# Kernel optimization log

Hardware: AMD Instinct MI355X
Metric: run time of the kernel (lower is better)

## Reference

```python
import jax, jax.numpy as jnp
import numpy as np

B, L, D = 16, 2048, 320          # batch, frames, stacked feature dim (80 mel * 4 reduction)
CODEBOOK_SIZE, CODEBOOK_DIM = 8192, 16


def setup_inputs() -> dict:
    key = jax.random.key(0)
    k1, k2, k3 = jax.random.split(key, 3)
    masked_target_values = jax.random.normal(k1, (B, L, D), dtype=jnp.float32)
    # xavier_uniform_ for shape (D, codebook_dim): bound = sqrt(6/(fan_in+fan_out))
    bound = np.sqrt(6.0 / (D + CODEBOOK_DIM)).astype(np.float32)
    project_mat = jax.random.uniform(k2, (D, CODEBOOK_DIM), dtype=jnp.float32,
                                     minval=-bound, maxval=bound)
    cb = jax.random.normal(k3, (CODEBOOK_SIZE, CODEBOOK_DIM), dtype=jnp.float32)
    codebook_norm = cb / jnp.maximum(jnp.linalg.norm(cb, axis=-1, keepdims=True), 1e-12)
    return {"masked_target_values": masked_target_values,
            "project_mat": project_mat,
            "codebook_norm": codebook_norm}


def reference(masked_target_values, project_mat, codebook_norm):
    # project: (B, L, D) @ (D, K) -> (B, L, K)
    targets = jnp.einsum('bld,dk->blk', masked_target_values, project_mat)
    # L2 normalize along last dim (torch F.normalize with eps=1e-12)
    targets_norm = targets / jnp.maximum(
        jnp.linalg.norm(targets, axis=-1, keepdims=True), 1e-12)
    x2 = jnp.sum(targets_norm * targets_norm, axis=-1, keepdims=True)      # (B, L, 1)
    c2 = jnp.sum(codebook_norm * codebook_norm, axis=-1)                   # (C,)
    xc = jnp.einsum('blk,ck->blc', targets_norm, codebook_norm)            # (B, L, C)
    d2 = jnp.maximum(x2 + c2[None, None, :] - 2.0 * xc, 0.0)
    vector_distances = jnp.sqrt(d2)
    labels = jnp.argmin(vector_distances, axis=-1)                         # (B, L) int
    return labels
```

## Files before the change

### kernel.cpp

```cpp
#include <hip/hip_runtime.h>
#include <cfloat>

#define TOKENS 32768
#define DIM    320
#define NCODE  8192
#define NSPLIT 8
#define SPAN   (NCODE / NSPLIT)
#define NTILE  (SPAN / 32)
#define CERT_UNITS 32u
#define FBWAVES 2048
#define PROW   20

typedef __attribute__((ext_vector_type(8)))  short short8;
typedef __attribute__((ext_vector_type(16))) float f32x16;
typedef unsigned short ushort_t;
typedef unsigned int   uint_t;

static __device__ __forceinline__ ushort_t f2bf(float f) {
    uint_t u = __float_as_uint(f);
    u += 0x7fffu + ((u >> 16) & 1u);
    return (ushort_t)(u >> 16);
}
static __device__ __forceinline__ float bf2f(ushort_t h) {
    return __uint_as_float(((uint_t)h) << 16);
}
static __device__ __forceinline__ uint_t pack2(ushort_t a, ushort_t b) {
    return (uint_t)a | ((uint_t)b << 16);
}
static __device__ __forceinline__ uint_t umaxu(uint_t a, uint_t b) { return a > b ? a : b; }
static __device__ __forceinline__ uint_t uminu(uint_t a, uint_t b) { return a < b ? a : b; }

__global__ __launch_bounds__(256) void prep_kernel(
    const float* __restrict__ x,
    const float* __restrict__ P,
    const float* __restrict__ cb,
    float* __restrict__ tn,
    float* __restrict__ x2o,
    float* __restrict__ c2o,
    ushort_t* __restrict__ tnpack,
    ushort_t* __restrict__ cbpack,
    int* __restrict__ cnt)
{
    __shared__ float Ps[DIM * PROW];
    int bid = blockIdx.x, tid = threadIdx.x;
    if (bid < TOKENS / 32) {
        const float4* P4 = (const float4*)P;
        #pragma unroll
        for (int i = 0; i < 5; ++i) {
            int idx = tid + i * 256;
            int row = idx >> 2, col = idx & 3;
            *(float4*)(Ps + row * PROW + col * 4) = P4[idx];
        }
        __syncthreads();

        int sub = tid & 7;
        int tok = bid * 32 + (tid >> 3);
        const float* xr = x + (size_t)tok * DIM;
        float acc[16];
        #pragma unroll
        for (int k = 0; k < 16; ++k) acc[k] = 0.f;

        for (int i = 0; i < 40; ++i) {
            int d = i * 8 + sub;
            float xv = xr[d];
            const float4* pr = (const float4*)(Ps + d * PROW);
            float4 p0 = pr[0], p1 = pr[1], p2 = pr[2], p3 = pr[3];
            acc[0] = fmaf(xv, p0.x, acc[0]);   acc[1] = fmaf(xv, p0.y, acc[1]);
            acc[2] = fmaf(xv, p0.z, acc[2]);   acc[3] = fmaf(xv, p0.w, acc[3]);
            acc[4] = fmaf(xv, p1.x, acc[4]);   acc[5] = fmaf(xv, p1.y, acc[5]);
            acc[6] = fmaf(xv, p1.z, acc[6]);   acc[7] = fmaf(xv, p1.w, acc[7]);
            acc[8] = fmaf(xv, p2.x, acc[8]);   acc[9] = fmaf(xv, p2.y, acc[9]);
            acc[10] = fmaf(xv, p2.z, acc[10]); acc[11] = fmaf(xv, p2.w, acc[11]);
            acc[12] = fmaf(xv, p3.x, acc[12]); acc[13] = fmaf(xv, p3.y, acc[13]);
            acc[14] = fmaf(xv, p3.z, acc[14]); acc[15] = fmaf(xv, p3.w, acc[15]);
        }
        #pragma unroll
        for (int m = 1; m <= 4; m <<= 1) {
            #pragma unroll
            for (int k = 0; k < 16; ++k)
                acc[k] += __shfl_xor(acc[k], m);
        }
        float ss = 0.f;
        #pragma unroll
        for (int k = 0; k < 16; ++k) ss = fmaf(acc[k], acc[k], ss);
        float nrm = fmaxf(sqrtf(ss), 1e-12f);
        float inv = 1.0f / nrm;
        float t[16];
        #pragma unroll
        for (int k = 0; k < 16; ++k) t[k] = acc[k] * inv;
        float xx = 0.f;
        #pragma unroll
        for (int k = 0; k < 16; ++k) xx = fmaf(t[k], t[k], xx);

        ushort_t hi[16], lo[16];
        #pragma unroll
        for (int k = 0; k < 16; ++k) {
            hi[k] = f2bf(t[k]);
            lo[k] = f2bf(t[k] - bf2f(hi[k]));
        }
        if (sub < 4) {
            float4* tf = (float4*)(tn + (size_t)tok * 16);
            tf[sub] = make_float4(t[4 * sub], t[4 * sub + 1],
                                  t[4 * sub + 2], t[4 * sub + 3]);
        }
        uint4* dst = (uint4*)(tnpack + (size_t)tok * 32);
        if (sub == 4) dst[0] = make_uint4(pack2(hi[0], hi[1]), pack2(hi[2], hi[3]),
                                          pack2(hi[4], hi[5]), pack2(hi[6], hi[7]));
        if (sub == 5) dst[1] = make_uint4(pack2(hi[8], hi[9]), pack2(hi[10], hi[11]),
                                          pack2(hi[12], hi[13]), pack2(hi[14], hi[15]));
        if (sub == 6) dst[2] = make_uint4(pack2(lo[0], lo[1]), pack2(lo[2], lo[3]),
                                          pack2(lo[4], lo[5]), pack2(lo[6], lo[7]));
        if (sub == 7) dst[3] = make_uint4(pack2(lo[8], lo[9]), pack2(lo[10], lo[11]),
                                          pack2(lo[12], lo[13]), pack2(lo[14], lo[15]));
        if (sub == 0) x2o[tok] = xx;
    } else {
        int j = (bid - TOKENS / 32) * 256 + tid;
        const float4* cr4 = (const float4*)(cb + (size_t)j * 16);
        float4 c0 = cr4[0], c1 = cr4[1], c2v = cr4[2], c3 = cr4[3];
        float c[16] = {c0.x, c0.y, c0.z, c0.w, c1.x, c1.y, c1.z, c1.w,
                       c2v.x, c2v.y, c2v.z, c2v.w, c3.x, c3.y, c3.z, c3.w};
        float s = 0.f;
        #pragma unroll
        for (int k = 0; k < 16; ++k) s = fmaf(c[k], c[k], s);
        c2o[j] = s;
        ushort_t hi[16], lo[16];
        #pragma unroll
        for (int k = 0; k < 16; ++k) {
            hi[k] = f2bf(c[k]);
            lo[k] = f2bf(c[k] - bf2f(hi[k]));
        }
        uint4* dst = (uint4*)(cbpack + (size_t)j * 32);
        dst[0] = make_uint4(pack2(hi[0], hi[1]), pack2(hi[2], hi[3]),
                            pack2(hi[4], hi[5]), pack2(hi[6], hi[7]));
        dst[1] = make_uint4(pack2(hi[8], hi[9]), pack2(hi[10], hi[11]),
                            pack2(hi[12], hi[13]), pack2(hi[14], hi[15]));
        dst[2] = make_uint4(pack2(lo[0], lo[1]), pack2(lo[2], lo[3]),
                            pack2(lo[4], lo[5]), pack2(lo[6], lo[7]));
        dst[3] = make_uint4(pack2(lo[8], lo[9]), pack2(lo[10], lo[11]),
                            pack2(lo[12], lo[13]), pack2(lo[14], lo[15]));
        if (j == 0) cnt[0] = 0;
    }
}

__global__ __launch_bounds__(256, 4) void search_kernel(
    const ushort_t* __restrict__ tnpack,
    const ushort_t* __restrict__ cbpack,
    uint_t* __restrict__ pp1,
    uint_t* __restrict__ pp2)
{
    int lane = threadIdx.x & 63;
    int wave = threadIdx.x >> 6;
    int half = lane >> 5;
    int l31  = lane & 31;
    int split = blockIdx.y;
    int tbase = blockIdx.x * 128 + wave * 32;

    const ushort_t* tp = tnpack + (size_t)(tbase + l31) * 32;
    short8 hiA = *(const short8*)(tp + half * 8);
    short8 loA = *(const short8*)(tp + 16 + half * 8);

    f32x16 zero = {};
    uint_t p1[16], p2[16];
    #pragma unroll
    for (int r = 0; r < 16; ++r) { p1[r] = 0u; p2[r] = 0u; }

    for (int t = 0; t < NTILE; ++t) {
        int crow = split * SPAN + t * 32 + l31;
        const ushort_t* cp = cbpack + (size_t)crow * 32;
        short8 hiB = *(const short8*)(cp + half * 8);
        short8 loB = *(const short8*)(cp + 16 + half * 8);

        f32x16 acc = __builtin_amdgcn_mfma_f32_32x32x16_bf16(hiA, hiB, zero, 0, 0, 0);
        acc = __builtin_amdgcn_mfma_f32_32x32x16_bf16(loA, hiB, acc, 0, 0, 0);
        acc = __builtin_amdgcn_mfma_f32_32x32x16_bf16(hiA, loB, acc, 0, 0, 0);

        uint_t inv = 8191u - (uint_t)crow;
        #pragma unroll
        for (int r = 0; r < 16; ++r) {
            float kf = fmaf(acc[r], 131072.0f, 131072.0f);
            uint_t ku = (uint_t)kf;
            uint_t p  = (ku << 13) | inv;
            p2[r] = umaxu(p2[r], uminu(p, p1[r]));
            p1[r] = umaxu(p1[r], p);
        }
    }

    #pragma unroll
    for (int mask = 1; mask <= 16; mask <<= 1) {
        #pragma unroll
        for (int r = 0; r < 16; ++r) {
            uint_t a1 = (uint_t)__shfl_xor((int)p1[r], mask);
            uint_t a2 = (uint_t)__shfl_xor((int)p2[r], mask);
            uint_t np2 = umaxu(uminu(p1[r], a1), umaxu(p2[r], a2));
            p1[r] = umaxu(p1[r], a1);
            p2[r] = np2;
        }
    }

    #pragma unroll
    for (int r = 0; r < 16; ++r) {
        if (l31 == r) {
            int mrow = (r & 3) + 8 * (r >> 2) + 4 * half;
            size_t slot = (size_t)split * TOKENS + (tbase + mrow);
            pp1[slot] = p1[r];
            pp2[slot] = p2[r];
        }
    }
}

__global__ __launch_bounds__(256) void reduce_flag_kernel(
    const uint_t* __restrict__ pp1,
    const uint_t* __restrict__ pp2,
    int* __restrict__ out,
    int* __restrict__ cnt,
    int* __restrict__ flag)
{
    int tok = blockIdx.x * 256 + threadIdx.x;
    uint_t p1 = pp1[tok], p2 = pp2[tok];
    #pragma unroll
    for (int s = 1; s < NSPLIT; ++s) {
        uint_t a1 = pp1[(size_t)s * TOKENS + tok];
        uint_t a2 = pp2[(size_t)s * TOKENS + tok];
        uint_t np2 = umaxu(uminu(p1, a1), umaxu(p2, a2));
        p1 = umaxu(p1, a1);
        p2 = np2;
    }
    out[tok] = 8191 - (int)(p1 & 8191u);
    if ((p1 >> 13) - (p2 >> 13) <= CERT_UNITS) {
        int pz = atomicAdd(cnt, 1);
        flag[pz] = tok;
    }
}

__global__ __launch_bounds__(256) void fallback_kernel(
    const float* __restrict__ tn,
    const float* __restrict__ x2i,
    const float* __restrict__ cb,
    const float* __restrict__ c2i,
    const int* __restrict__ cnt,
    const int* __restrict__ flag,
    int* __restrict__ out)
{
    int lane = threadIdx.x & 63;
    int wid = blockIdx.x * 4 + (threadIdx.x >> 6);
    int n = cnt[0];
    for (int f = wid; f < n; f += FBWAVES) {
        int tok = flag[f];
        const float4* tr = (const float4*)(tn + (size_t)tok * 16);
        float4 t0 = tr[0], t1 = tr[1], t2 = tr[2], t3 = tr[3];
        float a[16] = {t0.x, t0.y, t0.z, t0.w, t1.x, t1.y, t1.z, t1.w,
                       t2.x, t2.y, t2.z, t2.w, t3.x, t3.y, t3.z, t3.w};
        float xx = x2i[tok];
        float mn = FLT_MAX;
        int   id = 0x7fffffff;

        int j = lane;
        const float4* c4p = (const float4*)(cb + (size_t)j * 16);
        float4 n0 = c4p[0], n1 = c4p[1], n2 = c4p[2], n3 = c4p[3];
        float ncc = c2i[j];

        for (int jj = 0; jj < 128; ++jj) {
            float4 c0 = n0, c1 = n1, c2v = n2, c3 = n3;
            float cc = ncc;
            int cj = j;
            j += 64;
            if (jj < 127) {
                const float4* nx = (const float4*)(cb + (size_t)j * 16);
                n0 = nx[0]; n1 = nx[1]; n2 = nx[2]; n3 = nx[3];
                ncc = c2i[j];
            }
            float dot = 0.f;
            dot = fmaf(a[0], c0.x, dot);   dot = fmaf(a[1], c0.y, dot);
            dot = fmaf(a[2], c0.z, dot);   dot = fmaf(a[3], c0.w, dot);
            dot = fmaf(a[4], c1.x, dot);   dot = fmaf(a[5], c1.y, dot);
            dot = fmaf(a[6], c1.z, dot);   dot = fmaf(a[7], c1.w, dot);
            dot = fmaf(a[8], c2v.x, dot);  dot = fmaf(a[9], c2v.y, dot);
            dot = fmaf(a[10], c2v.z, dot); dot = fmaf(a[11], c2v.w, dot);
            dot = fmaf(a[12], c3.x, dot);  dot = fmaf(a[13], c3.y, dot);
            dot = fmaf(a[14], c3.z, dot);  dot = fmaf(a[15], c3.w, dot);
            float e = fmaf(-2.f, dot, xx + cc);
            if (e < mn) { mn = e; id = cj; }
        }
        #pragma unroll
        for (int mask = 1; mask <= 32; mask <<= 1) {
            float pmn = __shfl_xor(mn, mask);
            int   pid = __shfl_xor(id, mask);
            bool take = (pmn < mn) || (pmn == mn && pid < id);
            if (take) { mn = pmn; id = pid; }
        }
        if (lane == 0) out[tok] = id;
    }
}

extern "C" void kernel_launch(void* const* d_in, const int* in_sizes, int n_in,
                              void* d_out, int out_size, void* d_ws, size_t ws_size,
                              hipStream_t stream) {
    const float* x   = (const float*)d_in[0];
    const float* P   = (const float*)d_in[1];
    const float* cbn = (const float*)d_in[2];

    float* ws = (float*)d_ws;
    float*  tn   = ws;
    float*  x2   = tn + (size_t)TOKENS * 16;
    float*  c2   = x2 + TOKENS;
    uint_t* pp1  = (uint_t*)(c2 + NCODE);
    uint_t* pp2  = pp1 + (size_t)NSPLIT * TOKENS;
    int*    flag = (int*)(pp2 + (size_t)NSPLIT * TOKENS);
    int*    cnt  = flag + TOKENS;
    ushort_t* tnpack = (ushort_t*)(cnt + 16);
    ushort_t* cbpack = tnpack + (size_t)TOKENS * 32;
    int* labels = (int*)d_out;

    prep_kernel<<<TOKENS / 32 + NCODE / 256, 256, 0, stream>>>(
        x, P, cbn, tn, x2, c2, tnpack, cbpack, cnt);
    dim3 sg(TOKENS / 128, NSPLIT);
    search_kernel<<<sg, 256, 0, stream>>>(tnpack, cbpack, pp1, pp2);
    reduce_flag_kernel<<<TOKENS / 256, 256, 0, stream>>>(pp1, pp2, labels, cnt, flag);
    fallback_kernel<<<FBWAVES / 4, 256, 0, stream>>>(tn, x2, cbn, c2, cnt, flag, labels);
}
```

Baseline: 190.0 us.

## Fuse projection, MFMA search, merge and fallback into one per-block kernel

Replaces the four-kernel pipeline (prep, split search, reduce/flag, global fallback) with a small codebook pack kernel plus one fused kernel. Each block of 32 tokens projects and normalizes them into shared memory, then its four waves each scan a quarter of the codebook with bf16 hi/lo MFMA. The per-wave partials are merged in shared memory, and ambiguous tokens are resolved with an exact fp32 scan by the same block. This removes the global intermediates, atomics and extra launches. In exchange, each block now reads the whole packed codebook, and the grid holds fewer waves per token. The in-block fallback is serialized with syncthreads and can stall blocks that have many flagged tokens.

```diff
diff --git a/kernel.cpp b/kernel.cpp
--- a/kernel.cpp
+++ b/kernel.cpp
@@ -4,12 +4,9 @@
 #define TOKENS 32768
 #define DIM    320
 #define NCODE  8192
-#define NSPLIT 8
-#define SPAN   (NCODE / NSPLIT)
-#define NTILE  (SPAN / 32)
+#define PROW   20
+#define NTILE  64
 #define CERT_UNITS 32u
-#define FBWAVES 2048
-#define PROW   20
 
 typedef __attribute__((ext_vector_type(8)))  short short8;
 typedef __attribute__((ext_vector_type(16))) float f32x16;
@@ -30,20 +27,58 @@
 static __device__ __forceinline__ uint_t umaxu(uint_t a, uint_t b) { return a > b ? a : b; }
 static __device__ __forceinline__ uint_t uminu(uint_t a, uint_t b) { return a < b ? a : b; }
 
-__global__ __launch_bounds__(256) void prep_kernel(
+__global__ __launch_bounds__(256) void pack_kernel(
+    const float* __restrict__ cb,
+    float* __restrict__ c2o,
+    ushort_t* __restrict__ cbpack)
+{
+    int j = blockIdx.x * 256 + threadIdx.x;
+    const float4* cr4 = (const float4*)(cb + (size_t)j * 16);
+    float4 c0 = cr4[0], c1 = cr4[1], c2v = cr4[2], c3 = cr4[3];
+    float c[16] = {c0.x, c0.y, c0.z, c0.w, c1.x, c1.y, c1.z, c1.w,
+                   c2v.x, c2v.y, c2v.z, c2v.w, c3.x, c3.y, c3.z, c3.w};
+    float s = 0.f;
+    #pragma unroll
+    for (int k = 0; k < 16; ++k) s = fmaf(c[k], c[k], s);
+    c2o[j] = s;
+    ushort_t hi[16], lo[16];
+    #pragma unroll
+    for (int k = 0; k < 16; ++k) {
+        hi[k] = f2bf(c[k]);
+        lo[k] = f2bf(c[k] - bf2f(hi[k]));
+    }
+    uint4* dst = (uint4*)(cbpack + (size_t)j * 32);
+    dst[0] = make_uint4(pack2(hi[0], hi[1]), pack2(hi[2], hi[3]),
+                        pack2(hi[4], hi[5]), pack2(hi[6], hi[7]));
+    dst[1] = make_uint4(pack2(hi[8], hi[9]), pack2(hi[10], hi[11]),
+                        pack2(hi[12], hi[13]), pack2(hi[14], hi[15]));
+    dst[2] = make_uint4(pack2(lo[0], lo[1]), pack2(lo[2], lo[3]),
+                        pack2(lo[4], lo[5]), pack2(lo[6], lo[7]));
+    dst[3] = make_uint4(pack2(lo[8], lo[9]), pack2(lo[10], lo[11]),
+                        pack2(lo[12], lo[13]), pack2(lo[14], lo[15]));
+}
+
+__global__ __launch_bounds__(256, 4) void fused_kernel(
     const float* __restrict__ x,
     const float* __restrict__ P,
     const float* __restrict__ cb,
-    float* __restrict__ tn,
-    float* __restrict__ x2o,
-    float* __restrict__ c2o,
-    ushort_t* __restrict__ tnpack,
-    ushort_t* __restrict__ cbpack,
-    int* __restrict__ cnt)
+    const float* __restrict__ c2g,
+    const ushort_t* __restrict__ cbpack,
+    int* __restrict__ out)
 {
     __shared__ float Ps[DIM * PROW];
-    int bid = blockIdx.x, tid = threadIdx.x;
-    if (bid < TOKENS / 32) {
+    __shared__ ushort_t ApackS[32 * 32];
+    __shared__ float tnS[32 * 16];
+    __shared__ float x2S[32];
+    __shared__ uint_t mergeS[4][32][2];
+    __shared__ int flagS[36];
+    __shared__ float redE[4];
+    __shared__ int   redI[4];
+
+    int tid = threadIdx.x;
+    if (tid == 0) flagS[32] = 0;
+
+    {
         const float4* P4 = (const float4*)P;
         #pragma unroll
         for (int i = 0; i < 5; ++i) {
@@ -51,15 +86,17 @@
             int row = idx >> 2, col = idx & 3;
             *(float4*)(Ps + row * PROW + col * 4) = P4[idx];
         }
-        __syncthreads();
-
-        int sub = tid & 7;
-        int tok = bid * 32 + (tid >> 3);
+    }
+    __syncthreads();
+
+    int sub = tid & 7;
+    int tk  = tid >> 3;
+    int tok = blockIdx.x * 32 + tk;
+    {
         const float* xr = x + (size_t)tok * DIM;
         float acc[16];
         #pragma unroll
         for (int k = 0; k < 16; ++k) acc[k] = 0.f;
-
         for (int i = 0; i < 40; ++i) {
             int d = i * 8 + sub;
             float xv = xr[d];
@@ -99,11 +136,10 @@
             lo[k] = f2bf(t[k] - bf2f(hi[k]));
         }
         if (sub < 4) {
-            float4* tf = (float4*)(tn + (size_t)tok * 16);
-            tf[sub] = make_float4(t[4 * sub], t[4 * sub + 1],
-                                  t[4 * sub + 2], t[4 * sub + 3]);
-        }
-        uint4* dst = (uint4*)(tnpack + (size_t)tok * 32);
+            *(float4*)(tnS + tk * 16 + sub * 4) =
+                make_float4(t[4 * sub], t[4 * sub + 1], t[4 * sub + 2], t[4 * sub + 3]);
+        }
+        uint4* dst = (uint4*)(ApackS + tk * 32);
         if (sub == 4) dst[0] = make_uint4(pack2(hi[0], hi[1]), pack2(hi[2], hi[3]),
                                           pack2(hi[4], hi[5]), pack2(hi[6], hi[7]));
         if (sub == 5) dst[1] = make_uint4(pack2(hi[8], hi[9]), pack2(hi[10], hi[11]),
@@ -112,163 +148,97 @@
                                           pack2(lo[4], lo[5]), pack2(lo[6], lo[7]));
         if (sub == 7) dst[3] = make_uint4(pack2(lo[8], lo[9]), pack2(lo[10], lo[11]),
                                           pack2(lo[12], lo[13]), pack2(lo[14], lo[15]));
-        if (sub == 0) x2o[tok] = xx;
-    } else {
-        int j = (bid - TOKENS / 32) * 256 + tid;
-        const float4* cr4 = (const float4*)(cb + (size_t)j * 16);
-        float4 c0 = cr4[0], c1 = cr4[1], c2v = cr4[2], c3 = cr4[3];
-        float c[16] = {c0.x, c0.y, c0.z, c0.w, c1.x, c1.y, c1.z, c1.w,
-                       c2v.x, c2v.y, c2v.z, c2v.w, c3.x, c3.y, c3.z, c3.w};
-        float s = 0.f;
-        #pragma unroll
-        for (int k = 0; k < 16; ++k) s = fmaf(c[k], c[k], s);
-        c2o[j] = s;
-        ushort_t hi[16], lo[16];
-        #pragma unroll
-        for (int k = 0; k < 16; ++k) {
-            hi[k] = f2bf(c[k]);
-            lo[k] = f2bf(c[k] - bf2f(hi[k]));
-        }
-        uint4* dst = (uint4*)(cbpack + (size_t)j * 32);
-        dst[0] = make_uint4(pack2(hi[0], hi[1]), pack2(hi[2], hi[3]),
-                            pack2(hi[4], hi[5]), pack2(hi[6], hi[7]));
-        dst[1] = make_uint4(pack2(hi[8], hi[9]), pack2(hi[10], hi[11]),
-                            pack2(hi[12], hi[13]), pack2(hi[14], hi[15]));
-        dst[2] = make_uint4(pack2(lo[0], lo[1]), pack2(lo[2], lo[3]),
-                            pack2(lo[4], lo[5]), pack2(lo[6], lo[7]));
-        dst[3] = make_uint4(pack2(lo[8], lo[9]), pack2(lo[10], lo[11]),
-                            pack2(lo[12], lo[13]), pack2(lo[14], lo[15]));
-        if (j == 0) cnt[0] = 0;
-    }
-}
-
-__global__ __launch_bounds__(256, 4) void search_kernel(
-    const ushort_t* __restrict__ tnpack,
-    const ushort_t* __restrict__ cbpack,
-    uint_t* __restrict__ pp1,
-    uint_t* __restrict__ pp2)
-{
-    int lane = threadIdx.x & 63;
-    int wave = threadIdx.x >> 6;
+        if (sub == 0) x2S[tk] = xx;
+    }
+    __syncthreads();
+
+    int lane = tid & 63;
+    int wave = tid >> 6;
     int half = lane >> 5;
     int l31  = lane & 31;
-    int split = blockIdx.y;
-    int tbase = blockIdx.x * 128 + wave * 32;
-
-    const ushort_t* tp = tnpack + (size_t)(tbase + l31) * 32;
-    short8 hiA = *(const short8*)(tp + half * 8);
-    short8 loA = *(const short8*)(tp + 16 + half * 8);
-
-    f32x16 zero = {};
-    uint_t p1[16], p2[16];
-    #pragma unroll
-    for (int r = 0; r < 16; ++r) { p1[r] = 0u; p2[r] = 0u; }
-
-    for (int t = 0; t < NTILE; ++t) {
-        int crow = split * SPAN + t * 32 + l31;
-        const ushort_t* cp = cbpack + (size_t)crow * 32;
-        short8 hiB = *(const short8*)(cp + half * 8);
-        short8 loB = *(const short8*)(cp + 16 + half * 8);
-
-        f32x16 acc = __builtin_amdgcn_mfma_f32_32x32x16_bf16(hiA, hiB, zero, 0, 0, 0);
-        acc = __builtin_amdgcn_mfma_f32_32x32x16_bf16(loA, hiB, acc, 0, 0, 0);
-        acc = __builtin_amdgcn_mfma_f32_32x32x16_bf16(hiA, loB, acc, 0, 0, 0);
-
-        uint_t inv = 8191u - (uint_t)crow;
+    {
+        short8 hiA = *(const short8*)(ApackS + l31 * 32 + half * 8);
+        short8 loA = *(const short8*)(ApackS + l31 * 32 + 16 + half * 8);
+
+        f32x16 zero = {};
+        uint_t p1[16], p2[16];
+        #pragma unroll
+        for (int r = 0; r < 16; ++r) { p1[r] = 0u; p2[r] = 0u; }
+
+        for (int t = 0; t < NTILE; ++t) {
+            int crow = wave * (NTILE * 32) + t * 32 + l31;
+            const ushort_t* cp = cbpack + (size_t)crow * 32;
+            short8 hiB = *(const short8*)(cp + half * 8);
+            short8 loB = *(const short8*)(cp + 16 + half * 8);
+
+            f32x16 acc = __builtin_amdgcn_mfma_f32_32x32x16_bf16(hiA, hiB, zero, 0, 0, 0);
+            acc = __builtin_amdgcn_mfma_f32_32x32x16_bf16(loA, hiB, acc, 0, 0, 0);
+            acc = __builtin_amdgcn_mfma_f32_32x32x16_bf16(hiA, loB, acc, 0, 0, 0);
+
+            uint_t inv = 8191u - (uint_t)crow;
+            #pragma unroll
+            for (int r = 0; r < 16; ++r) {
+                float kf = fmaf(acc[r], 131072.0f, 131072.0f);
+                uint_t ku = (uint_t)kf;
+                uint_t p  = (ku << 13) | inv;
+                p2[r] = umaxu(p2[r], uminu(p, p1[r]));
+                p1[r] = umaxu(p1[r], p);
+            }
+        }
+        #pragma unroll
+        for (int mask = 1; mask <= 16; mask <<= 1) {
+            #pragma unroll
+            for (int r = 0; r < 16; ++r) {
+                uint_t a1 = (uint_t)__shfl_xor((int)p1[r], mask);
+                uint_t a2 = (uint_t)__shfl_xor((int)p2[r], mask);
+                uint_t np2 = umaxu(uminu(p1[r], a1), umaxu(p2[r], a2));
+                p1[r] = umaxu(p1[r], a1);
+                p2[r] = np2;
+            }
+        }
         #pragma unroll
         for (int r = 0; r < 16; ++r) {
-            float kf = fmaf(acc[r], 131072.0f, 131072.0f);
-            uint_t ku = (uint_t)kf;
-            uint_t p  = (ku << 13) | inv;
-            p2[r] = umaxu(p2[r], uminu(p, p1[r]));
-            p1[r] = umaxu(p1[r], p);
-        }
-    }
-
-    #pragma unroll
-    for (int mask = 1; mask <= 16; mask <<= 1) {
-        #pragma unroll
-        for (int r = 0; r < 16; ++r) {
-            uint_t a1 = (uint_t)__shfl_xor((int)p1[r], mask);
-            uint_t a2 = (uint_t)__shfl_xor((int)p2[r], mask);
-            uint_t np2 = umaxu(uminu(p1[r], a1), umaxu(p2[r], a2));
-            p1[r] = umaxu(p1[r], a1);
-            p2[r] = np2;
-        }
-    }
-
-    #pragma unroll
-    for (int r = 0; r < 16; ++r) {
-        if (l31 == r) {
-            int mrow = (r & 3) + 8 * (r >> 2) + 4 * half;
-            size_t slot = (size_t)split * TOKENS + (tbase + mrow);
-            pp1[slot] = p1[r];
-            pp2[slot] = p2[r];
-        }
-    }
-}
-
-__global__ __launch_bounds__(256) void reduce_flag_kernel(
-    const uint_t* __restrict__ pp1,
-    const uint_t* __restrict__ pp2,
-    int* __restrict__ out,
-    int* __restrict__ cnt,
-    int* __restrict__ flag)
-{
-    int tok = blockIdx.x * 256 + threadIdx.x;
-    uint_t p1 = pp1[tok], p2 = pp2[tok];
-    #pragma unroll
-    for (int s = 1; s < NSPLIT; ++s) {
-        uint_t a1 = pp1[(size_t)s * TOKENS + tok];
-        uint_t a2 = pp2[(size_t)s * TOKENS + tok];
-        uint_t np2 = umaxu(uminu(p1, a1), umaxu(p2, a2));
-        p1 = umaxu(p1, a1);
-        p2 = np2;
-    }
-    out[tok] = 8191 - (int)(p1 & 8191u);
-    if ((p1 >> 13) - (p2 >> 13) <= CERT_UNITS) {
-        int pz = atomicAdd(cnt, 1);
-        flag[pz] = tok;
-    }
-}
-
-__global__ __launch_bounds__(256) void fallback_kernel(
-    const float* __restrict__ tn,
-    const float* __restrict__ x2i,
-    const float* __restrict__ cb,
-    const float* __restrict__ c2i,
-    const int* __restrict__ cnt,
-    const int* __restrict__ flag,
-    int* __restrict__ out)
-{
-    int lane = threadIdx.x & 63;
-    int wid = blockIdx.x * 4 + (threadIdx.x >> 6);
-    int n = cnt[0];
-    for (int f = wid; f < n; f += FBWAVES) {
-        int tok = flag[f];
-        const float4* tr = (const float4*)(tn + (size_t)tok * 16);
-        float4 t0 = tr[0], t1 = tr[1], t2 = tr[2], t3 = tr[3];
-        float a[16] = {t0.x, t0.y, t0.z, t0.w, t1.x, t1.y, t1.z, t1.w,
-                       t2.x, t2.y, t2.z, t2.w, t3.x, t3.y, t3.z, t3.w};
-        float xx = x2i[tok];
+            if (l31 == r) {
+                int mrow = (r & 3) + 8 * (r >> 2) + 4 * half;
+                mergeS[wave][mrow][0] = p1[r];
+                mergeS[wave][mrow][1] = p2[r];
+            }
+        }
+    }
+    __syncthreads();
+
+    if (tid < 32) {
+        uint_t p1 = mergeS[0][tid][0], p2 = mergeS[0][tid][1];
+        #pragma unroll
+        for (int w = 1; w < 4; ++w) {
+            uint_t a1 = mergeS[w][tid][0];
+            uint_t a2 = mergeS[w][tid][1];
+            uint_t np2 = umaxu(uminu(p1, a1), umaxu(p2, a2));
+            p1 = umaxu(p1, a1);
+            p2 = np2;
+        }
+        if ((p1 >> 13) - (p2 >> 13) <= CERT_UNITS) {
+            int pz = atomicAdd(&flagS[32], 1);
+            flagS[pz] = tid;
+        } else {
+            out[blockIdx.x * 32 + tid] = 8191 - (int)(p1 & 8191u);
+        }
+    }
+    __syncthreads();
+
+    int nf = flagS[32];
+    for (int fi = 0; fi < nf; ++fi) {
+        int ftk = flagS[fi];
+        float a[16];
+        #pragma unroll
+        for (int k = 0; k < 16; ++k) a[k] = tnS[ftk * 16 + k];
+        float xx = x2S[ftk];
         float mn = FLT_MAX;
         int   id = 0x7fffffff;
-
-        int j = lane;
-        const float4* c4p = (const float4*)(cb + (size_t)j * 16);
-        float4 n0 = c4p[0], n1 = c4p[1], n2 = c4p[2], n3 = c4p[3];
-        float ncc = c2i[j];
-
-        for (int jj = 0; jj < 128; ++jj) {
-            float4 c0 = n0, c1 = n1, c2v = n2, c3 = n3;
-            float cc = ncc;
-            int cj = j;
-            j += 64;
-            if (jj < 127) {
-                const float4* nx = (const float4*)(cb + (size_t)j * 16);
-                n0 = nx[0]; n1 = nx[1]; n2 = nx[2]; n3 = nx[3];
-                ncc = c2i[j];
-            }
+        for (int c = 0; c < 32; ++c) {
+            int j = c * 256 + tid;
+            const float4* c4 = (const float4*)(cb + (size_t)j * 16);
+            float4 c0 = c4[0], c1 = c4[1], c2v = c4[2], c3 = c4[3];
             float dot = 0.f;
             dot = fmaf(a[0], c0.x, dot);   dot = fmaf(a[1], c0.y, dot);
             dot = fmaf(a[2], c0.z, dot);   dot = fmaf(a[3], c0.w, dot);
@@ -278,17 +248,26 @@
             dot = fmaf(a[10], c2v.z, dot); dot = fmaf(a[11], c2v.w, dot);
             dot = fmaf(a[12], c3.x, dot);  dot = fmaf(a[13], c3.y, dot);
             dot = fmaf(a[14], c3.z, dot);  dot = fmaf(a[15], c3.w, dot);
-            float e = fmaf(-2.f, dot, xx + cc);
-            if (e < mn) { mn = e; id = cj; }
+            float e = fmaf(-2.f, dot, xx + c2g[j]);
+            if (e < mn || (e == mn && j < id)) { mn = e; id = j; }
         }
         #pragma unroll
         for (int mask = 1; mask <= 32; mask <<= 1) {
             float pmn = __shfl_xor(mn, mask);
             int   pid = __shfl_xor(id, mask);
-            bool take = (pmn < mn) || (pmn == mn && pid < id);
-            if (take) { mn = pmn; id = pid; }
-        }
-        if (lane == 0) out[tok] = id;
+            if (pmn < mn || (pmn == mn && pid < id)) { mn = pmn; id = pid; }
+        }
+        if (lane == 0) { redE[wave] = mn; redI[wave] = id; }
+        __syncthreads();
+        if (tid == 0) {
+            #pragma unroll
+            for (int w = 1; w < 4; ++w) {
+                float pe = redE[w]; int pi = redI[w];
+                if (pe < mn || (pe == mn && pi < id)) { mn = pe; id = pi; }
+            }
+            out[blockIdx.x * 32 + ftk] = id;
+        }
+        __syncthreads();
     }
 }
 
@@ -299,22 +278,10 @@
     const float* P   = (const float*)d_in[1];
     const float* cbn = (const float*)d_in[2];
 
-    float* ws = (float*)d_ws;
-    float*  tn   = ws;
-    float*  x2   = tn + (size_t)TOKENS * 16;
-    float*  c2   = x2 + TOKENS;
-    uint_t* pp1  = (uint_t*)(c2 + NCODE);
-    uint_t* pp2  = pp1 + (size_t)NSPLIT * TOKENS;
-    int*    flag = (int*)(pp2 + (size_t)NSPLIT * TOKENS);
-    int*    cnt  = flag + TOKENS;
-    ushort_t* tnpack = (ushort_t*)(cnt + 16);
-    ushort_t* cbpack = tnpack + (size_t)TOKENS * 32;
+    float*    c2     = (float*)d_ws;
+    ushort_t* cbpack = (ushort_t*)(c2 + NCODE);
     int* labels = (int*)d_out;
 
-    prep_kernel<<<TOKENS / 32 + NCODE / 256, 256, 0, stream>>>(
-        x, P, cbn, tn, x2, c2, tnpack, cbpack, cnt);
-    dim3 sg(TOKENS / 128, NSPLIT);
-    search_kernel<<<sg, 256, 0, stream>>>(tnpack, cbpack, pp1, pp2);
-    reduce_flag_kernel<<<TOKENS / 256, 256, 0, stream>>>(pp1, pp2, labels, cnt, flag);
-    fallback_kernel<<<FBWAVES / 4, 256, 0, stream>>>(tn, x2, cbn, c2, cnt, flag, labels);
-}
+    pack_kernel<<<NCODE / 256, 256, 0, stream>>>(cbn, c2, cbpack);
+    fused_kernel<<<TOKENS / 32, 256, 0, stream>>>(x, P, cbn, c2, cbpack, labels);
+}
```

Result: faster. 174.8 us (-8.0%).
